# Performance work log

Measured on AMD Instinct MI355X. Metric: run time of the kernel, lower is better.

## Reference

```python
import jax, jax.numpy as jnp
import numpy as np

N = 100000   # nodes
E = 600000   # edges
D = 128      # input = hidden = output dim
L = 3        # GNN layers
C = 40       # num_classes
EPS = 1e-5   # BatchNorm eps


def setup_inputs() -> dict:
    key = jax.random.key(0)
    ks = jax.random.split(key, 8)
    x = jax.random.normal(ks[0], (N, D), jnp.float32)
    edge_index = jax.random.randint(ks[1], (2, E), 0, N, jnp.int32)
    # GCNConv weights per layer (Glorot-ish scale), bias zeros
    Ws = jax.random.normal(ks[2], (L, D, D), jnp.float32) / np.sqrt(D)
    bs = jnp.zeros((L, D), jnp.float32)
    # BatchNorm affine params
    gammas = jnp.ones((L, D), jnp.float32)
    betas = jnp.zeros((L, D), jnp.float32)
    # PReLU single slope per layer (torch default init 0.25)
    prelu_a = jnp.full((L,), 0.25, jnp.float32)
    # classification head: Linear(D,D) -> ReLU -> Linear(D,C)
    Wh1 = jax.random.normal(ks[3], (D, D), jnp.float32) / np.sqrt(D)
    bh1 = jnp.zeros((D,), jnp.float32)
    Wh2 = jax.random.normal(ks[4], (D, C), jnp.float32) / np.sqrt(D)
    bh2 = jnp.zeros((C,), jnp.float32)
    return dict(x=x, edge_index=edge_index, Ws=Ws, bs=bs, gammas=gammas,
                betas=betas, prelu_a=prelu_a, Wh1=Wh1, bh1=bh1, Wh2=Wh2, bh2=bh2)


def _gcn_conv(h, src, dst, norm, W, b):
    # PyG GCNConv: out_i = sum_{j->i} norm_ij * (x_j W) + b  (self-loops already in src/dst)
    m = (h @ W)[src] * norm[:, None]          # [E+N, D_out]
    return jax.ops.segment_sum(m, dst, num_segments=N) + b


def reference(x, edge_index, Ws, bs, gammas, betas, prelu_a, Wh1, bh1, Wh2, bh2):
    # add self-loops + symmetric normalization (computed once; same graph each layer)
    loops = jnp.arange(N, dtype=edge_index.dtype)
    src = jnp.concatenate([edge_index[0], loops])
    dst = jnp.concatenate([edge_index[1], loops])
    deg = jax.ops.segment_sum(jnp.ones_like(dst, jnp.float32), dst, num_segments=N)
    dinv = jax.lax.rsqrt(jnp.maximum(deg, 1.0))  # deg >= 1 thanks to self-loops
    norm = dinv[src] * dinv[dst]                 # [E+N]

    h = x
    for l in range(L):
        h = _gcn_conv(h, src, dst, norm, Ws[l], bs[l])
        # BatchNorm in training mode: batch statistics over nodes
        mu = h.mean(axis=0)
        var = h.var(axis=0)
        h = (h - mu) * jax.lax.rsqrt(var + EPS) * gammas[l] + betas[l]
        # PReLU
        h = jnp.where(h > 0, h, prelu_a[l] * h)

    embeddings = h
    logits = jax.nn.relu(embeddings @ Wh1 + bh1) @ Wh2 + bh2
    out = jnp.argmax(logits, axis=1)
    return embeddings, logits, out
```

## Files before the change

kernel.cpp:

```cpp
#include <hip/hip_runtime.h>
#include <hip/hip_bf16.h>
#include <cstddef>

#define N_NODES 100000
#define N_EDGES 600000
#define DD 128
#define LL 3
#define CC 40
#define BN_EPS 1e-5f

typedef __attribute__((ext_vector_type(8))) short bfrag;
typedef __attribute__((ext_vector_type(4))) float f32x4;

__device__ __forceinline__ float ldf(const void* p, long i, int f32) {
    return f32 ? ((const float*)p)[i] : __bfloat162float(((const __hip_bfloat16*)p)[i]);
}
__device__ __forceinline__ void stf(void* p, long i, float v, int f32) {
    if (f32) ((float*)p)[i] = v;
    else     ((__hip_bfloat16*)p)[i] = __float2bfloat16(v);
}

__device__ __forceinline__ unsigned short f2bf(float f) {
    unsigned u = __float_as_uint(f);
    unsigned r = (u + 0x7fffu + ((u >> 16) & 1u)) >> 16;
    return (unsigned short)r;
}
__device__ __forceinline__ float bf2f(unsigned short h) {
    return __uint_as_float(((unsigned)h) << 16);
}

__device__ __forceinline__ void gload_lds16(const unsigned short* g, unsigned short* l) {
    __builtin_amdgcn_global_load_lds((const __attribute__((address_space(1))) unsigned int*)g,
                                     (__attribute__((address_space(3))) unsigned int*)l, 16, 0, 0);
}

__global__ __launch_bounds__(256) void k_detect(const void* __restrict__ x, int* __restrict__ dflag) {
    __shared__ int s[256];
    int t = threadIdx.x;
    const __hip_bfloat16* xb = (const __hip_bfloat16*)x;
    int bad = 0;
    for (int i = t; i < 4096; i += 256) {
        float v = __bfloat162float(xb[i]);
        float a = fabsf(v);
        if (!(a < 1e6f)) bad++;
        else if (v != 0.f && a < 1e-30f) bad++;
    }
    s[t] = bad; __syncthreads();
    for (int off = 128; off > 0; off >>= 1) {
        if (t < off) s[t] += s[t + off];
        __syncthreads();
    }
    if (t == 0) *dflag = (s[0] > 64) ? 1 : 0;
}

__global__ __launch_bounds__(256) void k_packw(const void* __restrict__ Ws, const void* __restrict__ Wh1,
                                               unsigned short* __restrict__ Wp,
                                               const int* __restrict__ dflag) {
    int f = *dflag;
    int u = blockIdx.x * 256 + threadIdx.x;
    int mat = u >> 14;
    int r = u & 16383;
    int k = r >> 7, c = r & 127;
    float wv = (mat < 3) ? ldf(Ws, (long)mat * 16384 + r, f) : ldf(Wh1, r, f);
    unsigned short hi = f2bf(wv);
    float r1 = wv - bf2f(hi);
    unsigned short mid = f2bf(r1);
    float r2 = r1 - bf2f(mid);
    unsigned short lo = f2bf(r2);
    int n = c >> 4, ks = k >> 5, j = k & 7;
    int lanep = (c & 15) | (((k >> 3) & 3) << 4);
    long base = (long)mat * 49152 + (long)((n * 4 + ks) * 3) * 512 + lanep * 8 + j;
    Wp[base] = hi;
    Wp[base + 512] = mid;
    Wp[base + 1024] = lo;
}


__global__ __launch_bounds__(256) void k_init(int* cnt, int* fpos, int* rowptr, float* stats) {
    int i = blockIdx.x * 256 + threadIdx.x;
    if (i < N_NODES) { cnt[i] = 0; fpos[i] = 0; }
    if (i < 6 * DD) stats[i] = 0.f;
    if (i == 0) rowptr[N_NODES] = N_EDGES;
}

__global__ __launch_bounds__(256) void k_count(const int* __restrict__ ei, int* __restrict__ cnt) {
    int e = blockIdx.x * 256 + threadIdx.x;
    if (e < N_EDGES) atomicAdd(&cnt[ei[N_EDGES + e]], 1);
}

__global__ __launch_bounds__(256) void k_scan1(const int* __restrict__ cnt, int* __restrict__ rowptr,
                                               int* __restrict__ bsum, float* __restrict__ dinv) {
    __shared__ int s[256];
    int t = threadIdx.x;
    int i = blockIdx.x * 256 + t;
    int v = (i < N_NODES) ? cnt[i] : 0;
    if (i < N_NODES) dinv[i] = 1.f / sqrtf((float)(1 + v));
    s[t] = v; __syncthreads();
    for (int off = 1; off < 256; off <<= 1) {
        int x = (t >= off) ? s[t - off] : 0;
        __syncthreads();
        s[t] += x; __syncthreads();
    }
    if (i < N_NODES) rowptr[i] = s[t] - v;
    if (t == 255) bsum[blockIdx.x] = s[255];
}

__global__ __launch_bounds__(512) void k_scan2(int* bsum, int nb) {
    __shared__ int s[512];
    int t = threadIdx.x;
    int v = (t < nb) ? bsum[t] : 0;
    s[t] = v; __syncthreads();
    for (int off = 1; off < 512; off <<= 1) {
        int x = (t >= off) ? s[t - off] : 0;
        __syncthreads();
        s[t] += x; __syncthreads();
    }
    if (t < nb) bsum[t] = s[t] - v;
}

__global__ __launch_bounds__(256) void k_scan3(int* rowptr, const int* __restrict__ bsum) {
    int i = blockIdx.x * 256 + threadIdx.x;
    if (i < N_NODES) rowptr[i] += bsum[blockIdx.x];
}

__global__ __launch_bounds__(256) void k_fill(const int* __restrict__ ei, int* __restrict__ fpos,
                                              const int* __restrict__ rowptr, int2* __restrict__ adjw,
                                              const float* __restrict__ dinv) {
    int e = blockIdx.x * 256 + threadIdx.x;
    if (e < N_EDGES) {
        int s = ei[e];
        int d = ei[N_EDGES + e];
        int p = atomicAdd(&fpos[d], 1);
        adjw[rowptr[d] + p] = make_int2(s, __float_as_int(dinv[s]));
    }
}

__device__ __forceinline__ float4 load_row4(const void* __restrict__ src, long row, int q, int f) {
    if (f) {
        return ((const float4*)src)[row * 32 + q];
    } else {
        uint2 u = ((const uint2*)src)[row * 32 + q];
        float4 v;
        v.x = __uint_as_float(u.x << 16);
        v.y = __uint_as_float(u.x & 0xffff0000u);
        v.z = __uint_as_float(u.y << 16);
        v.w = __uint_as_float(u.y & 0xffff0000u);
        return v;
    }
}

__device__ __forceinline__ float4 bn4(float4 v, float4 sc, float4 sh, float al) {
    float y;
    y = fmaf(v.x, sc.x, sh.x); v.x = (y > 0.f) ? y : al * y;
    y = fmaf(v.y, sc.y, sh.y); v.y = (y > 0.f) ? y : al * y;
    y = fmaf(v.z, sc.z, sh.z); v.z = (y > 0.f) ? y : al * y;
    y = fmaf(v.w, sc.w, sh.w); v.w = (y > 0.f) ? y : al * y;
    return v;
}


__global__ __launch_bounds__(256) void k_agg(const void* __restrict__ src,
                                             const int* __restrict__ rowptr,
                                             const int2* __restrict__ adjw,
                                             const float* __restrict__ dinv,
                                             const float* __restrict__ stats,
                                             const void* __restrict__ gam,
                                             const void* __restrict__ bet,
                                             const void* __restrict__ pa,
                                             int bnl,
                                             float* __restrict__ outp,
                                             const int* __restrict__ dflag) {
    __shared__ float s_bn[260];
    int f = *dflag;
    int tid = threadIdx.x;
    bool useBN = (stats != nullptr);
    if (useBN) {
        if (tid < 128) {
            const float invn = 1.f / (float)N_NODES;
            float mean = stats[tid] * invn;
            float varv = stats[128 + tid] * invn - mean * mean;
            float s = ldf(gam, (long)bnl * DD + tid, f) / sqrtf(varv + BN_EPS);
            s_bn[tid] = s;
            s_bn[128 + tid] = ldf(bet, (long)bnl * DD + tid, f) - mean * s;
        }
        if (tid == 0) s_bn[256] = ldf(pa, bnl, f);
        __syncthreads();
    }

    int lane = tid & 63;
    int h = lane >> 5;
    int q = lane & 31;
    int i = blockIdx.x * 4 + (tid >> 6);
    if (i >= N_NODES) return;

    float4 sc = make_float4(1.f, 1.f, 1.f, 1.f);
    float4 sh = make_float4(0.f, 0.f, 0.f, 0.f);
    float al = 0.f;
    if (useBN) {
        sc = ((const float4*)s_bn)[q];
        sh = ((const float4*)(s_bn + 128))[q];
        al = s_bn[256];
    }

    float di = dinv[i];
    int e0 = rowptr[i], e1 = rowptr[i + 1];

    float a0 = 0.f, a1 = 0.f, a2 = 0.f, a3 = 0.f;
    if (h == 0) {
        float4 v = load_row4(src, i, q, f);
        if (useBN) v = bn4(v, sc, sh, al);
        a0 = di * v.x; a1 = di * v.y; a2 = di * v.z; a3 = di * v.w;
    }

    for (int base = e0; base < e1; base += 64) {
        int m = e1 - base; if (m > 64) m = 64;
        int2 aw = (lane < m) ? adjw[base + lane] : make_int2(0, 0);
        int ajl = aw.x;
        float wl = __int_as_float(aw.y);
        for (int t = 0; t < m; t += 4) {
            int s0 = t + h;     if (s0 > 63) s0 = 63;
            int s1 = t + 2 + h; if (s1 > 63) s1 = 63;
            int j0 = __shfl(ajl, s0), j1 = __shfl(ajl, s1);
            float w0 = __shfl(wl, s0), w1 = __shfl(wl, s1);
            float4 v0 = load_row4(src, j0, q, f);
            float4 v1 = load_row4(src, j1, q, f);
            if (useBN) {
                v0 = bn4(v0, sc, sh, al);
                v1 = bn4(v1, sc, sh, al);
            }
            a0 += w0 * v0.x + w1 * v1.x;
            a1 += w0 * v0.y + w1 * v1.y;
            a2 += w0 * v0.z + w1 * v1.z;
            a3 += w0 * v0.w + w1 * v1.w;
        }
    }

    a0 += __shfl_xor(a0, 32);
    a1 += __shfl_xor(a1, 32);
    a2 += __shfl_xor(a2, 32);
    a3 += __shfl_xor(a3, 32);

    if (h == 0) {
        float4 r = make_float4(di * a0, di * a1, di * a2, di * a3);
        ((float4*)outp)[(size_t)i * 32 + q] = r;
    }
}


__global__ __launch_bounds__(256, 2) void k_gemm2(const float* __restrict__ A,
                                                  const unsigned short* __restrict__ Wp,
                                                  const void* __restrict__ bias, long boff,
                                                  const float* __restrict__ statsA,
                                                  const void* __restrict__ gam,
                                                  const void* __restrict__ bet,
                                                  const void* __restrict__ pa, int bnl,
                                                  float* __restrict__ stats,
                                                  float* __restrict__ Cout,
                                                  void* __restrict__ embp, int relu,
                                                  const int* __restrict__ dflag) {
    __shared__ unsigned short Wl[24576];
    int f = *dflag;
    int tid = threadIdx.x;
    int lane = tid & 63;
    int w = tid >> 6;

    #pragma unroll
    for (int u = 0; u < 12; ++u) {
        int chunk = w * 12 + u;
        gload_lds16(Wp + chunk * 512 + lane * 8, &Wl[chunk * 512]);
    }

    int lr = lane & 15;
    int lg = lane >> 4;
    int rowbase = blockIdx.x * 128 + w * 32;

    float bcol[8];
    #pragma unroll
    for (int n = 0; n < 8; ++n)
        bcol[n] = bias ? ldf(bias, boff + n * 16 + lr, f) : 0.f;

    float alA = statsA ? ldf(pa, bnl, f) : 0.f;
    const float invn = 1.f / (float)N_NODES;

    bfrag ah[2][4], am[2][4], alo[2][4];
    const float4* A4 = (const float4*)A;
    #pragma unroll
    for (int ks = 0; ks < 4; ++ks) {
        int k0 = ks * 32 + lg * 8;
        float bs_[8], bh_[8];
        if (statsA) {
            #pragma unroll
            for (int e = 0; e < 8; ++e) {
                int c = k0 + e;
                float mean = statsA[c] * invn;
                float varv = statsA[128 + c] * invn - mean * mean;
                float s = ldf(gam, (long)bnl * DD + c, f) / sqrtf(varv + BN_EPS);
                bs_[e] = s;
                bh_[e] = ldf(bet, (long)bnl * DD + c, f) - mean * s;
            }
        }
        #pragma unroll
        for (int s = 0; s < 2; ++s) {
            int row = rowbase + s * 16 + lr;
            float xv[8];
            if (row < N_NODES) {
                long bi = (long)row * 32 + (k0 >> 2);
                float4 x0 = A4[bi], x1 = A4[bi + 1];
                xv[0] = x0.x; xv[1] = x0.y; xv[2] = x0.z; xv[3] = x0.w;
                xv[4] = x1.x; xv[5] = x1.y; xv[6] = x1.z; xv[7] = x1.w;
            } else {
                #pragma unroll
                for (int e = 0; e < 8; ++e) xv[e] = 0.f;
            }
            if (statsA) {
                #pragma unroll
                for (int e = 0; e < 8; ++e) {
                    float y = fmaf(xv[e], bs_[e], bh_[e]);
                    xv[e] = (y > 0.f) ? y : alA * y;
                }
            }
            bfrag hfr, mfr, lfr;
            #pragma unroll
            for (int e = 0; e < 8; ++e) {
                unsigned short hb2 = f2bf(xv[e]);
                float r1 = xv[e] - bf2f(hb2);
                unsigned short mb2 = f2bf(r1);
                float r2 = r1 - bf2f(mb2);
                hfr[e] = (short)hb2;
                mfr[e] = (short)mb2;
                lfr[e] = (short)f2bf(r2);
            }
            ah[s][ks] = hfr;
            am[s][ks] = mfr;
            alo[s][ks] = lfr;
            if (embp && row < N_NODES) {
                if (f) {
                    ((float4*)embp)[(long)row * 32 + (k0 >> 2)]     = make_float4(xv[0], xv[1], xv[2], xv[3]);
                    ((float4*)embp)[(long)row * 32 + (k0 >> 2) + 1] = make_float4(xv[4], xv[5], xv[6], xv[7]);
                } else {
                    uint4 pk;
                    pk.x = (unsigned)(unsigned short)hfr[0] | ((unsigned)(unsigned short)hfr[1] << 16);
                    pk.y = (unsigned)(unsigned short)hfr[2] | ((unsigned)(unsigned short)hfr[3] << 16);
                    pk.z = (unsigned)(unsigned short)hfr[4] | ((unsigned)(unsigned short)hfr[5] << 16);
                    pk.w = (unsigned)(unsigned short)hfr[6] | ((unsigned)(unsigned short)hfr[7] << 16);
                    ((uint4*)embp)[(long)row * 16 + (k0 >> 3)] = pk;
                }
            }
        }
    }

    f32x4 acc[2][8];
    #pragma unroll
    for (int s = 0; s < 2; ++s)
        #pragma unroll
        for (int n = 0; n < 8; ++n) acc[s][n] = (f32x4){0.f, 0.f, 0.f, 0.f};

    __syncthreads();

    #pragma unroll
    for (int nn = 0; nn < 4; ++nn) {
        int n = nn;
        bfrag bh[4], bm[4], bl[4];
        #pragma unroll
        for (int ks = 0; ks < 4; ++ks) {
            int base = ((nn * 4 + ks) * 3) * 512 + lane * 8;
            bh[ks] = *(const bfrag*)&Wl[base];
            bm[ks] = *(const bfrag*)&Wl[base + 512];
            bl[ks] = *(const bfrag*)&Wl[base + 1024];
        }
        #pragma unroll
        for (int ks = 0; ks < 4; ++ks) {
            #pragma unroll
            for (int s = 0; s < 2; ++s) {
                acc[s][n] = __builtin_amdgcn_mfma_f32_16x16x32_bf16(ah[s][ks],  bh[ks], acc[s][n], 0, 0, 0);
                acc[s][n] = __builtin_amdgcn_mfma_f32_16x16x32_bf16(am[s][ks],  bh[ks], acc[s][n], 0, 0, 0);
                acc[s][n] = __builtin_amdgcn_mfma_f32_16x16x32_bf16(ah[s][ks],  bm[ks], acc[s][n], 0, 0, 0);
                acc[s][n] = __builtin_amdgcn_mfma_f32_16x16x32_bf16(am[s][ks],  bm[ks], acc[s][n], 0, 0, 0);
                acc[s][n] = __builtin_amdgcn_mfma_f32_16x16x32_bf16(alo[s][ks], bh[ks], acc[s][n], 0, 0, 0);
                acc[s][n] = __builtin_amdgcn_mfma_f32_16x16x32_bf16(ah[s][ks],  bl[ks], acc[s][n], 0, 0, 0);
            }
        }
    }

    __syncthreads();
    #pragma unroll
    for (int u = 0; u < 12; ++u) {
        int chunk = w * 12 + u;
        gload_lds16(Wp + 24576 + chunk * 512 + lane * 8, &Wl[chunk * 512]);
    }
    __syncthreads();

    #pragma unroll
    for (int nn = 0; nn < 4; ++nn) {
        int n = 4 + nn;
        bfrag bh[4], bm[4], bl[4];
        #pragma unroll
        for (int ks = 0; ks < 4; ++ks) {
            int base = ((nn * 4 + ks) * 3) * 512 + lane * 8;
            bh[ks] = *(const bfrag*)&Wl[base];
            bm[ks] = *(const bfrag*)&Wl[base + 512];
            bl[ks] = *(const bfrag*)&Wl[base + 1024];
        }
        #pragma unroll
        for (int ks = 0; ks < 4; ++ks) {
            #pragma unroll
            for (int s = 0; s < 2; ++s) {
                acc[s][n] = __builtin_amdgcn_mfma_f32_16x16x32_bf16(ah[s][ks],  bh[ks], acc[s][n], 0, 0, 0);
                acc[s][n] = __builtin_amdgcn_mfma_f32_16x16x32_bf16(am[s][ks],  bh[ks], acc[s][n], 0, 0, 0);
                acc[s][n] = __builtin_amdgcn_mfma_f32_16x16x32_bf16(ah[s][ks],  bm[ks], acc[s][n], 0, 0, 0);
                acc[s][n] = __builtin_amdgcn_mfma_f32_16x16x32_bf16(am[s][ks],  bm[ks], acc[s][n], 0, 0, 0);
                acc[s][n] = __builtin_amdgcn_mfma_f32_16x16x32_bf16(alo[s][ks], bh[ks], acc[s][n], 0, 0, 0);
                acc[s][n] = __builtin_amdgcn_mfma_f32_16x16x32_bf16(ah[s][ks],  bl[ks], acc[s][n], 0, 0, 0);
            }
        }
    }

    int rowst[2][4]; bool rv[2][4];
    #pragma unroll
    for (int s = 0; s < 2; ++s)
        #pragma unroll
        for (int reg = 0; reg < 4; ++reg) {
            rowst[s][reg] = rowbase + s * 16 + lg * 4 + reg;
            rv[s][reg] = rowst[s][reg] < N_NODES;
        }

    float ls[8], lq[8];
    #pragma unroll
    for (int n = 0; n < 8; ++n) { ls[n] = 0.f; lq[n] = 0.f; }

    #pragma unroll
    for (int s = 0; s < 2; ++s)
        #pragma unroll
        for (int n = 0; n < 8; ++n) {
            int colb = n * 16 + lr;
            #pragma unroll
            for (int reg = 0; reg < 4; ++reg) {
                if (rv[s][reg]) {
                    float o = acc[s][n][reg] + bcol[n];
                    if (relu) o = fmaxf(o, 0.f);
                    Cout[(long)rowst[s][reg] * 128 + colb] = o;
                    ls[n] += o;
                    lq[n] += o * o;
                }
            }
        }

    if (stats) {
        #pragma unroll
        for (int n = 0; n < 8; ++n) {
            ls[n] += __shfl_xor(ls[n], 16);
            ls[n] += __shfl_xor(ls[n], 32);
            lq[n] += __shfl_xor(lq[n], 16);
            lq[n] += __shfl_xor(lq[n], 32);
        }
        __syncthreads();
        float* red = (float*)Wl;
        if (lane < 16) {
            #pragma unroll
            for (int n = 0; n < 8; ++n) {
                red[w * 256 + n * 16 + lane] = ls[n];
                red[w * 256 + 128 + n * 16 + lane] = lq[n];
            }
        }
        __syncthreads();
        float t = red[tid] + red[256 + tid] + red[512 + tid] + red[768 + tid];
        atomicAdd(&stats[tid], t);
    }
}


__global__ __launch_bounds__(256) void k_head(const float* __restrict__ Hd, const void* __restrict__ W2,
                                              const void* __restrict__ b2,
                                              void* __restrict__ out_base,
                                              const int* __restrict__ dflag) {
    __shared__ float Wl[128][40];
    __shared__ float bl[40];
    __shared__ float rv[32][8];
    __shared__ int ri[32][8];
    int f = *dflag;
    int tid = threadIdx.x;
    for (int u = tid; u < 128 * 40; u += 256) Wl[u / 40][u % 40] = ldf(W2, u, f);
    if (tid < 40) bl[tid] = ldf(b2, tid, f);
    __syncthreads();
    int rl = tid >> 3, g = tid & 7;
    long r = (long)blockIdx.x * 32 + rl;
    float acc[5];
    #pragma unroll
    for (int j = 0; j < 5; ++j) acc[j] = bl[g * 5 + j];
    for (int k = 0; k < 128; ++k) {
        float h = Hd[r * 128 + k];
        #pragma unroll
        for (int j = 0; j < 5; ++j) acc[j] += h * Wl[k][g * 5 + j];
    }
    float best = acc[0]; int bi = 0;
    #pragma unroll
    for (int j = 1; j < 5; ++j)
        if (acc[j] > best) { best = acc[j]; bi = j; }
    const long LOG_OFF = (long)N_NODES * DD;
    const long ARG_OFF = (long)N_NODES * (DD + CC);
    #pragma unroll
    for (int j = 0; j < 5; ++j) stf(out_base, LOG_OFF + r * 40 + g * 5 + j, acc[j], f);
    rv[rl][g] = best; ri[rl][g] = g * 5 + bi;
    __syncthreads();
    if (tid < 32) {
        long row = (long)blockIdx.x * 32 + tid;
        float bb = rv[tid][0]; int bbi = ri[tid][0];
        #pragma unroll
        for (int g2 = 1; g2 < 8; ++g2)
            if (rv[tid][g2] > bb) { bb = rv[tid][g2]; bbi = ri[tid][g2]; }
        stf(out_base, ARG_OFF + row, (float)bbi, f);
    }
}


extern "C" void kernel_launch(void* const* d_in, const int* in_sizes, int n_in,
                              void* d_out, int out_size, void* d_ws, size_t ws_size,
                              hipStream_t stream) {
    const void* x   = d_in[0];
    const int* ei   = (const int*)d_in[1];
    const void* Ws  = d_in[2];
    const void* bs  = d_in[3];
    const void* gam = d_in[4];
    const void* bet = d_in[5];
    const void* pa  = d_in[6];
    const void* Wh1 = d_in[7];
    const void* bh1 = d_in[8];
    const void* Wh2 = d_in[9];
    const void* bh2 = d_in[10];

    char* w = (char*)d_ws;
    int* cnt     = (int*)w;    w += sizeof(int) * N_NODES;
    int* fpos    = (int*)w;    w += sizeof(int) * N_NODES;
    int* rowptr  = (int*)w;    w += sizeof(int) * (N_NODES + 4);
    int2* adjw   = (int2*)w;   w += sizeof(int2) * N_EDGES;
    int* bsum    = (int*)w;    w += sizeof(int) * 512;
    int* dflag   = (int*)w;    w += sizeof(int) * 4;
    float* dinv  = (float*)w;  w += sizeof(float) * N_NODES;
    float* stats = (float*)w;  w += sizeof(float) * (6 * DD);
    unsigned short* Wp = (unsigned short*)w; w += sizeof(unsigned short) * 4 * 49152;
    float* bufA  = (float*)w;  w += sizeof(float) * (size_t)N_NODES * DD;
    float* bufB  = (float*)w;  w += sizeof(float) * (size_t)N_NODES * DD;

    const int scanBlocks = (N_NODES + 255) / 256;
    const int edgeBlocks = (N_EDGES + 255) / 256;
    const int gemmBlocks = (N_NODES + 127) / 128;
    const int aggBlocks  = (N_NODES + 3) / 4;

    k_detect<<<1, 256, 0, stream>>>(x, dflag);
    k_packw<<<256, 256, 0, stream>>>(Ws, Wh1, Wp, dflag);
    k_init<<<scanBlocks, 256, 0, stream>>>(cnt, fpos, rowptr, stats);
    k_count<<<edgeBlocks, 256, 0, stream>>>(ei, cnt);
    k_scan1<<<scanBlocks, 256, 0, stream>>>(cnt, rowptr, bsum, dinv);
    k_scan2<<<1, 512, 0, stream>>>(bsum, scanBlocks);
    k_scan3<<<scanBlocks, 256, 0, stream>>>(rowptr, bsum);
    k_fill<<<edgeBlocks, 256, 0, stream>>>(ei, fpos, rowptr, adjw, dinv);

    for (int l = 0; l < LL; ++l) {
        const void* src = (l == 0) ? x : (const void*)bufB;
        const float* st = (l == 0) ? nullptr : (stats + (l - 1) * 256);
        k_agg<<<aggBlocks, 256, 0, stream>>>(src, rowptr, adjw, dinv, st, gam, bet, pa,
                                             l - 1, bufA, dflag);
        k_gemm2<<<gemmBlocks, 256, 0, stream>>>(bufA, Wp + (size_t)l * 49152, bs, (long)l * DD,
                                                nullptr, gam, bet, pa, 0,
                                                stats + l * 256, bufB, nullptr, 0, dflag);
    }

    k_gemm2<<<gemmBlocks, 256, 0, stream>>>(bufB, Wp + (size_t)3 * 49152, bh1, 0,
                                            stats + 2 * 256, gam, bet, pa, 2,
                                            nullptr, bufA, d_out, 1, dflag);
    k_head<<<(N_NODES / 32), 256, 0, stream>>>(bufA, Wh2, bh2, d_out, dflag);
}
```

Measured before the change: 624.4 us.

## Load GEMM weight fragments directly from global memory instead of staging in LDS

The GEMM kernel no longer stages the packed bf16 weight fragments into a 48 KB LDS buffer in two halves with barriers. Each wave now reads its B fragments straight from global memory, relying on L1/L2 caching since every block reads the same weights. LDS use drops to a small reduction buffer, so launch bounds are raised to allow three blocks per SM. The cost is more global and cache traffic per wave, and possibly higher latency on the weight loads.

Measured after the change: 884.7 us. +41.7%, slower.

```diff
diff --git a/kernel.cpp b/kernel.cpp
--- a/kernel.cpp
+++ b/kernel.cpp
@@ -27,11 +27,6 @@
 }
 __device__ __forceinline__ float bf2f(unsigned short h) {
     return __uint_as_float(((unsigned)h) << 16);
-}
-
-__device__ __forceinline__ void gload_lds16(const unsigned short* g, unsigned short* l) {
-    __builtin_amdgcn_global_load_lds((const __attribute__((address_space(1))) unsigned int*)g,
-                                     (__attribute__((address_space(3))) unsigned int*)l, 16, 0, 0);
 }
 
 __global__ __launch_bounds__(256) void k_detect(const void* __restrict__ x, int* __restrict__ dflag) {
@@ -247,7 +242,7 @@
 }
 
 
-__global__ __launch_bounds__(256, 2) void k_gemm2(const float* __restrict__ A,
+__global__ __launch_bounds__(256, 3) void k_gemm2(const float* __restrict__ A,
                                                   const unsigned short* __restrict__ Wp,
                                                   const void* __restrict__ bias, long boff,
                                                   const float* __restrict__ statsA,
@@ -258,17 +253,11 @@
                                                   float* __restrict__ Cout,
                                                   void* __restrict__ embp, int relu,
                                                   const int* __restrict__ dflag) {
-    __shared__ unsigned short Wl[24576];
+    __shared__ float red[1024];
     int f = *dflag;
     int tid = threadIdx.x;
     int lane = tid & 63;
     int w = tid >> 6;
-
-    #pragma unroll
-    for (int u = 0; u < 12; ++u) {
-        int chunk = w * 12 + u;
-        gload_lds16(Wp + chunk * 512 + lane * 8, &Wl[chunk * 512]);
-    }
 
     int lr = lane & 15;
     int lg = lane >> 4;
@@ -355,51 +344,16 @@
         #pragma unroll
         for (int n = 0; n < 8; ++n) acc[s][n] = (f32x4){0.f, 0.f, 0.f, 0.f};
 
-    __syncthreads();
-
-    #pragma unroll
-    for (int nn = 0; nn < 4; ++nn) {
-        int n = nn;
+    const bfrag* Wf = (const bfrag*)Wp;
+    #pragma unroll
+    for (int n = 0; n < 8; ++n) {
         bfrag bh[4], bm[4], bl[4];
         #pragma unroll
         for (int ks = 0; ks < 4; ++ks) {
-            int base = ((nn * 4 + ks) * 3) * 512 + lane * 8;
-            bh[ks] = *(const bfrag*)&Wl[base];
-            bm[ks] = *(const bfrag*)&Wl[base + 512];
-            bl[ks] = *(const bfrag*)&Wl[base + 1024];
-        }
-        #pragma unroll
-        for (int ks = 0; ks < 4; ++ks) {
-            #pragma unroll
-            for (int s = 0; s < 2; ++s) {
-                acc[s][n] = __builtin_amdgcn_mfma_f32_16x16x32_bf16(ah[s][ks],  bh[ks], acc[s][n], 0, 0, 0);
-                acc[s][n] = __builtin_amdgcn_mfma_f32_16x16x32_bf16(am[s][ks],  bh[ks], acc[s][n], 0, 0, 0);
-                acc[s][n] = __builtin_amdgcn_mfma_f32_16x16x32_bf16(ah[s][ks],  bm[ks], acc[s][n], 0, 0, 0);
-                acc[s][n] = __builtin_amdgcn_mfma_f32_16x16x32_bf16(am[s][ks],  bm[ks], acc[s][n], 0, 0, 0);
-                acc[s][n] = __builtin_amdgcn_mfma_f32_16x16x32_bf16(alo[s][ks], bh[ks], acc[s][n], 0, 0, 0);
-                acc[s][n] = __builtin_amdgcn_mfma_f32_16x16x32_bf16(ah[s][ks],  bl[ks], acc[s][n], 0, 0, 0);
-            }
-        }
-    }
-
-    __syncthreads();
-    #pragma unroll
-    for (int u = 0; u < 12; ++u) {
-        int chunk = w * 12 + u;
-        gload_lds16(Wp + 24576 + chunk * 512 + lane * 8, &Wl[chunk * 512]);
-    }
-    __syncthreads();
-
-    #pragma unroll
-    for (int nn = 0; nn < 4; ++nn) {
-        int n = 4 + nn;
-        bfrag bh[4], bm[4], bl[4];
-        #pragma unroll
-        for (int ks = 0; ks < 4; ++ks) {
-            int base = ((nn * 4 + ks) * 3) * 512 + lane * 8;
-            bh[ks] = *(const bfrag*)&Wl[base];
-            bm[ks] = *(const bfrag*)&Wl[base + 512];
-            bl[ks] = *(const bfrag*)&Wl[base + 1024];
+            int base = ((n * 4 + ks) * 3) * 64 + lane;
+            bh[ks] = Wf[base];
+            bm[ks] = Wf[base + 64];
+            bl[ks] = Wf[base + 128];
         }
         #pragma unroll
         for (int ks = 0; ks < 4; ++ks) {
@@ -453,8 +407,6 @@
             lq[n] += __shfl_xor(lq[n], 16);
             lq[n] += __shfl_xor(lq[n], 32);
         }
-        __syncthreads();
-        float* red = (float*)Wl;
         if (lane < 16) {
             #pragma unroll
             for (int n = 0; n < 8; ++n) {
```
